# Kernel tuning notes

Hardware: AMD Instinct MI355X
Metric: run time of the kernel (lower is better)

Reference implementation:

```python
import jax, jax.numpy as jnp
import numpy as np

EMB = 768
HEADS = 12
HEAD_DIM = EMB // HEADS
LN_EPS = 1e-5


def _layernorm(x, g, b):
    mu = jnp.mean(x, axis=-1, keepdims=True)
    var = jnp.mean(jnp.square(x - mu), axis=-1, keepdims=True)
    return (x - mu) * jax.lax.rsqrt(var + LN_EPS) * g + b


def _att_block(x, ln_g, ln_b, w_qkv, b_qkv, w_proj, b_proj):
    # x: [b, n, e]
    B, N, E = x.shape
    h, d = HEADS, HEAD_DIM
    qkv = _layernorm(x, ln_g, ln_b) @ w_qkv.T + b_qkv          # [b, n, 3e]
    # einops 'b n (h d qkv)': last axis factors as (h, d, 3), qkv innermost
    qkv = qkv.reshape(B, N, h, d, 3)
    qkv = jnp.moveaxis(qkv, (4, 2), (0, 2))                    # [3, b, h, n, d]
    q, k, v = qkv[0], qkv[1], qkv[2]
    scale = d ** (-0.5)
    # NOTE: original code DIVIDES by scale (= multiplies by sqrt(d)) -- faithful
    scores = jnp.einsum('bhqd,bhkd->bhqk', q, k) / scale       # [b, h, n, n]
    attn = jax.nn.softmax(scores, axis=-1)
    out = jnp.einsum('bhqk,bhkd->bhqd', attn, v)               # [b, h, n, d]
    out = out.transpose(0, 2, 1, 3).reshape(B, N, E)           # [b, n, e]
    return x + out @ w_proj.T + b_proj


def setup_inputs() -> dict:
    key = jax.random.key(0)
    ks = jax.random.split(key, 8)
    B, N, E = 2, 2048, EMB
    s = E ** (-0.5)
    return {
        'modal1': jax.random.normal(ks[0], (B, N, E), jnp.float32),
        'modal2': jax.random.normal(ks[1], (B, N, E), jnp.float32),
        'ln1_g': jnp.ones((E,), jnp.float32),
        'ln1_b': jnp.zeros((E,), jnp.float32),
        'w_qkv1': jax.random.normal(ks[2], (3 * E, E), jnp.float32) * s,
        'b_qkv1': jnp.zeros((3 * E,), jnp.float32),
        'w_proj1': jax.random.normal(ks[3], (E, E), jnp.float32) * s,
        'b_proj1': jnp.zeros((E,), jnp.float32),
        'ln2_g': jnp.ones((E,), jnp.float32),
        'ln2_b': jnp.zeros((E,), jnp.float32),
        'w_qkv2': jax.random.normal(ks[4], (3 * E, E), jnp.float32) * s,
        'b_qkv2': jnp.zeros((3 * E,), jnp.float32),
        'w_proj2': jax.random.normal(ks[5], (E, E), jnp.float32) * s,
        'b_proj2': jnp.zeros((E,), jnp.float32),
    }


def reference(modal1, modal2, ln1_g, ln1_b, w_qkv1, b_qkv1, w_proj1, b_proj1,
              ln2_g, ln2_b, w_qkv2, b_qkv2, w_proj2, b_proj2):
    out1 = _att_block(modal1, ln1_g, ln1_b, w_qkv1, b_qkv1, w_proj1, b_proj1)
    out2 = _att_block(modal2, ln2_g, ln2_b, w_qkv2, b_qkv2, w_proj2, b_proj2)
    return (out1, out2)
```

## Files before the change

kernel.cpp:

```cpp
#include <hip/hip_runtime.h>
#include <hip/hip_bf16.h>


typedef unsigned short u16;
typedef unsigned int   u32;
typedef __attribute__((ext_vector_type(4)))  float floatx4;
typedef __attribute__((ext_vector_type(16))) float floatx16;
typedef __attribute__((ext_vector_type(8)))  short shortx8;
typedef __attribute__((ext_vector_type(2)))  unsigned int uintx2;

#define EMB   768
#define SEQ   2048
#define NHEAD 12
#define HDIM  64
#define RPM   4096
#define NROW  8192
#define NUNIT 48
#define KTS   4096
#define CS_SCALE 11.5415603271f

__device__ __forceinline__ float bf2f(u16 h) {
  union { u32 u; float f; } v; v.u = ((u32)h) << 16; return v.f;
}
__device__ __forceinline__ u16 f2bf(float f) {
  union { float f; u32 u; } v; v.f = f;
  u32 r = v.u + 0x7fffu + ((v.u >> 16) & 1u);
  return (u16)(r >> 16);
}
__device__ __forceinline__ u32 cvtpk_bf16(float a, float b) {
  u32 r;
  asm("v_cvt_pk_bf16_f32 %0, %1, %2" : "=v"(r) : "v"(a), "v"(b));
  return r;
}
__device__ __forceinline__ void swap_halves(u32 a, u32 b, u32& x, u32& y) {
#if __has_builtin(__builtin_amdgcn_permlane32_swap)
  uintx2 r = __builtin_amdgcn_permlane32_swap(a, b, false, false);
  x = r.x; y = r.y;
#else
  u32 ax = (u32)__shfl_xor((int)a, 32);
  u32 bx = (u32)__shfl_xor((int)b, 32);
  bool h = (threadIdx.x & 32) != 0;
  x = h ? bx : a;
  y = h ? b : ax;
#endif
}

__global__ __launch_bounds__(256) void k_pre(
    const float* __restrict__ wq1, const float* __restrict__ wq2,
    u16* __restrict__ wh, u16* __restrict__ wl,
    const float* __restrict__ x1, const float* __restrict__ x2,
    const float* __restrict__ g1, const float* __restrict__ b1,
    const float* __restrict__ g2, const float* __restrict__ b2,
    u16* __restrict__ xn_hi, u16* __restrict__ xn_lo)
{
  int bx = blockIdx.x;
  int t = threadIdx.x;
  if (bx < 4608) {
    int modal = bx / 2304, rowp = bx % 2304;
    int typ = rowp / 768, hd = rowp % 768;
    const float* W = (modal ? wq2 : wq1) + (size_t)(hd * 3 + typ) * EMB;
    size_t dst = (size_t)bx * EMB;
    #pragma unroll
    for (int i = 0; i < 3; ++i) {
      int e = t + i * 256;
      float v = W[e];
      u16 h = f2bf(v);
      wh[dst + e] = h;
      wl[dst + e] = f2bf(v - bf2f(h));
    }
  } else {
    int row = bx - 4608;
    int modal = row >> 12;
    const float* x = modal ? x2 : x1;
    const float* g = modal ? g2 : g1;
    const float* bb = modal ? b2 : b1;
    int r = row & (RPM - 1);
    const float* xr = x + (size_t)r * EMB;
    float v0 = xr[t], v1 = xr[t + 256], v2 = xr[t + 512];
    float s = v0 + v1 + v2;
    float s2 = v0 * v0 + v1 * v1 + v2 * v2;
    #pragma unroll
    for (int m = 1; m < 64; m <<= 1) { s += __shfl_xor(s, m); s2 += __shfl_xor(s2, m); }
    __shared__ float ls[4], ls2[4];
    int w = t >> 6;
    if ((t & 63) == 0) { ls[w] = s; ls2[w] = s2; }
    __syncthreads();
    s = ls[0] + ls[1] + ls[2] + ls[3];
    s2 = ls2[0] + ls2[1] + ls2[2] + ls2[3];
    float mu = s * (1.0f / EMB);
    float var = s2 * (1.0f / EMB) - mu * mu;
    float rs = rsqrtf(var + 1e-5f);
    size_t base = (size_t)row * EMB;
    float vv[3] = { v0, v1, v2 };
    #pragma unroll
    for (int i = 0; i < 3; ++i) {
      int e = t + i * 256;
      float xn = (vv[i] - mu) * rs * g[e] + bb[e];
      u16 h = f2bf(xn);
      xn_hi[base + e] = h;
      xn_lo[base + e] = f2bf(xn - bf2f(h));
    }
  }
}

__global__ __launch_bounds__(256) void prep_wp(
    const float* __restrict__ wp1, const float* __restrict__ wp2,
    u16* __restrict__ wh)
{
  int bx = blockIdx.x;
  int modal = bx / 768, row = bx % 768;
  const float* W = (modal ? wp2 : wp1) + (size_t)row * EMB;
  size_t dst = (size_t)bx * EMB;
  int t = threadIdx.x;
  #pragma unroll
  for (int i = 0; i < 3; ++i) {
    int e = t + i * 256;
    wh[dst + e] = f2bf(W[e]);
  }
}

__global__ __launch_bounds__(256) void k_qkv(
    const u16* __restrict__ xn_hi, const u16* __restrict__ xn_lo,
    const u16* __restrict__ wqh, const u16* __restrict__ wql,
    const float* __restrict__ bq1, const float* __restrict__ bq2,
    u16* __restrict__ q_hi, u16* __restrict__ q_lo,
    u16* __restrict__ k_hi, u16* __restrict__ k_lo,
    u16* __restrict__ vT)
{
  int mt = blockIdx.x, ntile = blockIdx.y, modal = blockIdx.z;
  const float* BQ = modal ? bq2 : bq1;
  int typ = ntile / 6;
  int hd0 = (ntile % 6) * 128;

  __shared__ __align__(16) u16 As_hi[2][128 * 32], Wh[2][128 * 32],
                               As_lo[2][128 * 32], Wl[2][128 * 32];

  int tid = threadIdx.x, lane = tid & 63, w = tid >> 6;
  int wm = (w >> 1) * 64, wn = (w & 1) * 64;
  int lc = lane & 15, lq = lane >> 4;

  int srow = lane >> 2;
  int schunk = ((lane & 3) ^ (srow & 3)) << 3;

  floatx4 acc[4][4] = {};
  const u16* aH = xn_hi + (size_t)(modal * RPM + mt * 128) * EMB;
  const u16* aL = xn_lo + (size_t)(modal * RPM + mt * 128) * EMB;
  const u16* wH = wqh + (size_t)(modal * 2304 + typ * 768 + hd0) * EMB;
  const u16* wL = wql + (size_t)(modal * 2304 + typ * 768 + hd0) * EMB;

  auto stage = [&](int buf, int k0) {
    if (typ != 2) {
      #pragma unroll
      for (int c = 0; c < 8; ++c) {
        int seg = w * 8 + c;
        int tile = seg >> 3, segin = seg & 7;
        size_t off = (size_t)(segin * 16 + srow) * EMB + k0 + schunk;
        const u16* src; u16* dstb;
        if (tile == 0)      { src = aH + off; dstb = &As_hi[buf][0]; }
        else if (tile == 1) { src = wH + off; dstb = &Wh[buf][0]; }
        else if (tile == 2) { src = aL + off; dstb = &As_lo[buf][0]; }
        else                { src = wL + off; dstb = &Wl[buf][0]; }
        __builtin_amdgcn_global_load_lds(
            (const __attribute__((address_space(1))) unsigned int*)src,
            (__attribute__((address_space(3))) unsigned int*)(dstb + segin * 512), 16, 0, 0);
      }
    } else {
      #pragma unroll
      for (int c = 0; c < 4; ++c) {
        int seg = w * 4 + c;
        int tile = seg >> 3, segin = seg & 7;
        size_t off = (size_t)(segin * 16 + srow) * EMB + k0 + schunk;
        const u16* src; u16* dstb;
        if (tile == 0) { src = aH + off; dstb = &As_hi[buf][0]; }
        else           { src = wH + off; dstb = &Wh[buf][0]; }
        __builtin_amdgcn_global_load_lds(
            (const __attribute__((address_space(1))) unsigned int*)src,
            (__attribute__((address_space(3))) unsigned int*)(dstb + segin * 512), 16, 0, 0);
      }
    }
  };

  stage(0, 0);
  for (int kk = 0; kk < 24; ++kk) {
    int cur = kk & 1;
    bool more = (kk + 1 < 24);
    if (more) stage(cur ^ 1, (kk + 1) * 32);
    if (typ != 2) {
      if (more) asm volatile("s_waitcnt vmcnt(8)" ::: "memory");
      else      asm volatile("s_waitcnt vmcnt(0)" ::: "memory");
    } else {
      if (more) asm volatile("s_waitcnt vmcnt(4)" ::: "memory");
      else      asm volatile("s_waitcnt vmcnt(0)" ::: "memory");
    }
    __builtin_amdgcn_s_barrier();
    __builtin_amdgcn_sched_barrier(0);

    shortx8 ah[4], al[4], whf[4], wlf[4];
    int rsw = lc & 3;
    int ca = (lq ^ rsw) << 3;
    #pragma unroll
    for (int i = 0; i < 4; ++i) {
      int ra = wm + i * 16 + lc, rw = wn + i * 16 + lc;
      ah[i]  = *(const shortx8*)&As_hi[cur][ra * 32 + ca];
      whf[i] = *(const shortx8*)&Wh[cur][rw * 32 + ca];
      if (typ != 2) {
        al[i]  = *(const shortx8*)&As_lo[cur][ra * 32 + ca];
        wlf[i] = *(const shortx8*)&Wl[cur][rw * 32 + ca];
      }
    }
    #pragma unroll
    for (int i = 0; i < 4; ++i)
      #pragma unroll
      for (int jn = 0; jn < 4; ++jn) {
        acc[i][jn] = __builtin_amdgcn_mfma_f32_16x16x32_bf16(ah[i], whf[jn], acc[i][jn], 0, 0, 0);
        if (typ != 2) {
          acc[i][jn] = __builtin_amdgcn_mfma_f32_16x16x32_bf16(al[i], whf[jn], acc[i][jn], 0, 0, 0);
          acc[i][jn] = __builtin_amdgcn_mfma_f32_16x16x32_bf16(ah[i], wlf[jn], acc[i][jn], 0, 0, 0);
        }
      }
    asm volatile("s_waitcnt lgkmcnt(0)" ::: "memory");
    __builtin_amdgcn_s_barrier();
    __builtin_amdgcn_sched_barrier(0);
  }

  #pragma unroll
  for (int i = 0; i < 4; ++i) {
    int mrow0 = mt * 128 + wm + i * 16 + lq * 4;
    #pragma unroll
    for (int jn = 0; jn < 4; ++jn) {
      int colp = hd0 + wn + jn * 16 + lc;
      int h = colp >> 6, d = colp & 63;
      float bias = BQ[colp * 3 + typ];
      #pragma unroll
      for (int r = 0; r < 4; ++r) {
        int mrow = mrow0 + r;
        int b = mrow >> 11, nq = mrow & (SEQ - 1);
        int uu = modal * 24 + b * 12 + h;
        float val = acc[i][jn][r] + bias;
        if (typ == 0) {
          val *= CS_SCALE;
          size_t o = ((size_t)uu * SEQ + nq) * HDIM + d;
          u16 hh = f2bf(val); q_hi[o] = hh; q_lo[o] = f2bf(val - bf2f(hh));
        } else if (typ == 1) {
          size_t o = ((size_t)uu * SEQ + nq) * HDIM + d;
          u16 hh = f2bf(val); k_hi[o] = hh; k_lo[o] = f2bf(val - bf2f(hh));
        } else {
          vT[((size_t)uu * HDIM + d) * SEQ + nq] = f2bf(val);
        }
      }
    }
  }
}

__global__ __launch_bounds__(256, 3) void k_attn(
    const u16* __restrict__ q_hi, const u16* __restrict__ q_lo,
    const u16* __restrict__ k_hi, const u16* __restrict__ k_lo,
    const u16* __restrict__ vT, u16* __restrict__ attn_out)
{
  int id = blockIdx.x + (blockIdx.y << 4);
  int xcd = id & 7, j = id >> 3;
  int u = xcd * 6 + (j >> 4);
  int qt = j & 15;

  __shared__ __align__(16) u16 lds[2][3 * KTS];

  int tid = threadIdx.x, lane = tid & 63, w = tid >> 6;
  int col = lane & 31, hi = lane >> 5;
  int swz = (col & 7) << 4;

  shortx8 qh[4], qlo[4];
  {
    size_t qb = ((size_t)u * SEQ + qt * 128 + w * 32 + col) * HDIM + hi * 8;
    #pragma unroll
    for (int s = 0; s < 4; ++s) {
      qh[s]  = *(const shortx8*)(q_hi + qb + s * 16);
      qlo[s] = *(const shortx8*)(q_lo + qb + s * 16);
    }
  }

  int lrow = lane >> 3;
  int lcol = ((lane & 7) ^ lrow) << 3;
  const u16* kh_src = k_hi + (size_t)u * SEQ * HDIM;
  const u16* kl_src = k_lo + (size_t)u * SEQ * HDIM;
  const u16* v_src  = vT  + (size_t)u * HDIM * SEQ;

  auto stage = [&](int buf, int kc) {
    #pragma unroll
    for (int c = 0; c < 6; ++c) {
      int seg = w * 6 + c;
      int tile = seg >> 3, segin = seg & 7;
      u16* dst = &lds[buf][tile * KTS + segin * 512];
      const u16* src;
      if (tile == 0)      src = kh_src + (size_t)(kc + segin * 8 + lrow) * HDIM + lcol;
      else if (tile == 1) src = kl_src + (size_t)(kc + segin * 8 + lrow) * HDIM + lcol;
      else                src = v_src  + (size_t)(segin * 8 + lrow) * SEQ + kc + lcol;
      __builtin_amdgcn_global_load_lds(
          (const __attribute__((address_space(1))) unsigned int*)src,
          (__attribute__((address_space(3))) unsigned int*)dst, 16, 0, 0);
    }
  };

  floatx16 O0 = {}, O1 = {};
  float m_r = -1e30f, lsum = 0.0f;
  const float THR = 8.0f;

  stage(0, 0);
  __syncthreads();

  for (int t = 0; t < SEQ / 64; ++t) {
    int cur = t & 1;
    if (t + 1 < SEQ / 64) stage(cur ^ 1, (t + 1) * 64);

    const char* Kh = (const char*)&lds[cur][0];
    const char* Kl = (const char*)&lds[cur][KTS];
    const char* Vt = (const char*)&lds[cur][2 * KTS];

    floatx16 S0 = {}, S1 = {};
    __builtin_amdgcn_s_setprio(1);
    #pragma unroll
    for (int s = 0; s < 4; ++s) {
      int cb = (s * 32 + hi * 16) ^ swz;
      shortx8 kf0 = *(const shortx8*)(Kh + col * 128 + cb);
      shortx8 kl0 = *(const shortx8*)(Kl + col * 128 + cb);
      shortx8 kf1 = *(const shortx8*)(Kh + (32 + col) * 128 + cb);
      shortx8 kl1 = *(const shortx8*)(Kl + (32 + col) * 128 + cb);
      S0 = __builtin_amdgcn_mfma_f32_32x32x16_bf16(kf0, qh[s],  S0, 0, 0, 0);
      S1 = __builtin_amdgcn_mfma_f32_32x32x16_bf16(kf1, qh[s],  S1, 0, 0, 0);
      S0 = __builtin_amdgcn_mfma_f32_32x32x16_bf16(kf0, qlo[s], S0, 0, 0, 0);
      S1 = __builtin_amdgcn_mfma_f32_32x32x16_bf16(kf1, qlo[s], S1, 0, 0, 0);
      S0 = __builtin_amdgcn_mfma_f32_32x32x16_bf16(kl0, qh[s],  S0, 0, 0, 0);
      S1 = __builtin_amdgcn_mfma_f32_32x32x16_bf16(kl1, qh[s],  S1, 0, 0, 0);
    }
    __builtin_amdgcn_s_setprio(0);

    float tm[16];
    #pragma unroll
    for (int r = 0; r < 16; ++r) tm[r] = fmaxf(S0[r], S1[r]);
    #pragma unroll
    for (int st = 8; st >= 1; st >>= 1)
      #pragma unroll
      for (int i = 0; i < st; ++i) tm[i] = fmaxf(tm[i], tm[i + st]);
    float mx = tm[0];
    mx = fmaxf(mx, __shfl_xor(mx, 32));

    if (!__all(mx <= m_r + THR)) {
      float mn = fmaxf(m_r, mx);
      float alpha = __builtin_amdgcn_exp2f(m_r - mn);
      m_r = mn;
      lsum *= alpha;
      #pragma unroll
      for (int r = 0; r < 16; ++r) {
        int qsrc = (r & 3) + 8 * (r >> 2) + 4 * hi;
        union { float f; int i; } a; a.f = alpha;
        a.i = __builtin_amdgcn_ds_bpermute(qsrc << 2, a.i);
        O0[r] *= a.f; O1[r] *= a.f;
      }
    }

    __builtin_amdgcn_s_setprio(1);
    #pragma unroll
    for (int ks = 0; ks < 4; ++ks) {
      const int h2 = ks & 1;
      float ee[8];
      #pragma unroll
      for (int i = 0; i < 8; ++i) {
        float sv = (ks < 2) ? S0[h2 * 8 + i] : S1[h2 * 8 + i];
        ee[i] = __builtin_amdgcn_exp2f(sv - m_r);
      }
      lsum += ((ee[0] + ee[1]) + (ee[2] + ee[3])) + ((ee[4] + ee[5]) + (ee[6] + ee[7]));
      u32 A = cvtpk_bf16(ee[0], ee[1]);
      u32 B = cvtpk_bf16(ee[2], ee[3]);
      u32 C = cvtpk_bf16(ee[4], ee[5]);
      u32 D = cvtpk_bf16(ee[6], ee[7]);
      u32 w0, w1, w2, w3;
      swap_halves(A, C, w0, w2);
      swap_halves(B, D, w1, w3);
      union { u32 uu[4]; shortx8 ss; } pk_;
      pk_.uu[0] = w0; pk_.uu[1] = w1; pk_.uu[2] = w2; pk_.uu[3] = w3;
      int cb = (ks * 32 + hi * 16) ^ swz;
      shortx8 v0 = *(const shortx8*)(Vt + col * 128 + cb);
      shortx8 v1 = *(const shortx8*)(Vt + (32 + col) * 128 + cb);
      O0 = __builtin_amdgcn_mfma_f32_32x32x16_bf16(pk_.ss, v0, O0, 0, 0, 0);
      O1 = __builtin_amdgcn_mfma_f32_32x32x16_bf16(pk_.ss, v1, O1, 0, 0, 0);
    }
    __builtin_amdgcn_s_setprio(0);

    __syncthreads();
  }

  float lt = lsum + __shfl_xor(lsum, 32);
  float rl = __builtin_amdgcn_rcpf(lt);
  int modal = u / 24, b = (u / 12) & 1, h = u % 12;
  size_t obase = ((size_t)(modal * RPM + b * SEQ + qt * 128 + w * 32)) * EMB + h * 64 + col;
  #pragma unroll
  for (int r = 0; r < 16; ++r) {
    int ql_ = (r & 3) + 8 * (r >> 2) + 4 * hi;
    union { float f; int i; } a; a.f = rl;
    a.i = __builtin_amdgcn_ds_bpermute(ql_ << 2, a.i);
    size_t ob = obase + (size_t)ql_ * EMB;
    attn_out[ob]      = f2bf(O0[r] * a.f);
    attn_out[ob + 32] = f2bf(O1[r] * a.f);
  }
}

__global__ __launch_bounds__(256) void k_proj(
    const u16* __restrict__ ao, const u16* __restrict__ wph,
    const float* __restrict__ x1, const float* __restrict__ x2,
    const float* __restrict__ bp1, const float* __restrict__ bp2,
    float* __restrict__ out)
{
  int mt = blockIdx.x, ntile = blockIdx.y, modal = blockIdx.z;
  const float* BP = modal ? bp2 : bp1;
  const float* x  = modal ? x2 : x1;

  __shared__ __align__(16) u16 As[2][64 * 32], Ws[2][128 * 32];
  int tid = threadIdx.x, lane = tid & 63, w = tid >> 6;
  int wm = (w >> 1) * 32, wn = (w & 1) * 64;
  int lc = lane & 15, lq = lane >> 4;

  int srow = lane >> 2;
  int schunk = ((lane & 3) ^ (srow & 3)) << 3;

  floatx4 acc[2][4] = {};
  const u16* aP = ao  + (size_t)(modal * RPM + mt * 64) * EMB;
  const u16* wP = wph + (size_t)(modal * 768 + ntile * 128) * EMB;

  auto stage = [&](int buf, int k0) {
    #pragma unroll
    for (int c = 0; c < 3; ++c) {
      int seg = w * 3 + c;
      const u16* src; u16* dst;
      if (seg < 4) {
        src = aP + (size_t)(seg * 16 + srow) * EMB + k0 + schunk;
        dst = &As[buf][0] + seg * 512;
      } else {
        int s2 = seg - 4;
        src = wP + (size_t)(s2 * 16 + srow) * EMB + k0 + schunk;
        dst = &Ws[buf][0] + s2 * 512;
      }
      __builtin_amdgcn_global_load_lds(
          (const __attribute__((address_space(1))) unsigned int*)src,
          (__attribute__((address_space(3))) unsigned int*)dst, 16, 0, 0);
    }
  };

  stage(0, 0);
  for (int kk = 0; kk < 24; ++kk) {
    int cur = kk & 1;
    bool more = (kk + 1 < 24);
    if (more) stage(cur ^ 1, (kk + 1) * 32);
    if (more) asm volatile("s_waitcnt vmcnt(3)" ::: "memory");
    else      asm volatile("s_waitcnt vmcnt(0)" ::: "memory");
    __builtin_amdgcn_s_barrier();
    __builtin_amdgcn_sched_barrier(0);

    int ca = (lq ^ (lc & 3)) << 3;
    shortx8 af[2], wf[4];
    #pragma unroll
    for (int i = 0; i < 2; ++i) af[i] = *(const shortx8*)&As[cur][(wm + i * 16 + lc) * 32 + ca];
    #pragma unroll
    for (int i = 0; i < 4; ++i) wf[i] = *(const shortx8*)&Ws[cur][(wn + i * 16 + lc) * 32 + ca];
    #pragma unroll
    for (int i = 0; i < 2; ++i)
      #pragma unroll
      for (int jn = 0; jn < 4; ++jn)
        acc[i][jn] = __builtin_amdgcn_mfma_f32_16x16x32_bf16(af[i], wf[jn], acc[i][jn], 0, 0, 0);
    asm volatile("s_waitcnt lgkmcnt(0)" ::: "memory");
    __builtin_amdgcn_s_barrier();
    __builtin_amdgcn_sched_barrier(0);
  }

  #pragma unroll
  for (int i = 0; i < 2; ++i) {
    int mrow0 = mt * 64 + wm + i * 16 + lq * 4;
    #pragma unroll
    for (int jn = 0; jn < 4; ++jn) {
      int col = ntile * 128 + wn + jn * 16 + lc;
      float bias = BP[col];
      #pragma unroll
      for (int r = 0; r < 4; ++r) {
        int mrow = mrow0 + r;
        float val = acc[i][jn][r] + bias + x[(size_t)mrow * EMB + col];
        out[((size_t)(modal * RPM + mrow)) * EMB + col] = val;
      }
    }
  }
}

extern "C" void kernel_launch(void* const* d_in, const int* in_sizes, int n_in,
                              void* d_out, int out_size, void* d_ws, size_t ws_size,
                              hipStream_t stream) {
  const float* modal1 = (const float*)d_in[0];
  const float* modal2 = (const float*)d_in[1];
  const float* ln1_g  = (const float*)d_in[2];
  const float* ln1_b  = (const float*)d_in[3];
  const float* w_qkv1 = (const float*)d_in[4];
  const float* b_qkv1 = (const float*)d_in[5];
  const float* w_proj1= (const float*)d_in[6];
  const float* b_proj1= (const float*)d_in[7];
  const float* ln2_g  = (const float*)d_in[8];
  const float* ln2_b  = (const float*)d_in[9];
  const float* w_qkv2 = (const float*)d_in[10];
  const float* b_qkv2 = (const float*)d_in[11];
  const float* w_proj2= (const float*)d_in[12];
  const float* b_proj2= (const float*)d_in[13];
  float* out = (float*)d_out;

  const size_t BUFE = (size_t)NROW * EMB;
  const size_t WQE  = (size_t)2 * 2304 * EMB;
  u16* xn_hi = (u16*)d_ws;
  u16* xn_lo = xn_hi + BUFE;
  u16* q_hi  = xn_lo + BUFE;
  u16* q_lo  = q_hi + BUFE;
  u16* k_hi  = q_lo + BUFE;
  u16* k_lo  = k_hi + BUFE;
  u16* vT    = k_lo + BUFE;
  u16* wq_h  = vT + BUFE;
  u16* wq_l  = wq_h + WQE;
  u16* attn  = xn_hi;
  u16* wp_h  = q_lo;

  k_pre<<<4608 + NROW, 256, 0, stream>>>(w_qkv1, w_qkv2, wq_h, wq_l,
                                         modal1, modal2, ln1_g, ln1_b, ln2_g, ln2_b,
                                         xn_hi, xn_lo);
  dim3 g2(32, 18, 2);
  k_qkv<<<g2, 256, 0, stream>>>(xn_hi, xn_lo, wq_h, wq_l, b_qkv1, b_qkv2,
                                q_hi, q_lo, k_hi, k_lo, vT);
  dim3 g3(16, 48);
  k_attn<<<g3, 256, 0, stream>>>(q_hi, q_lo, k_hi, k_lo, vT, attn);
  prep_wp<<<1536, 256, 0, stream>>>(w_proj1, w_proj2, wp_h);
  dim3 g4(64, 6, 2);
  k_proj<<<g4, 256, 0, stream>>>(attn, wp_h, modal1, modal2, b_proj1, b_proj2, out);
}
```

Before: 345.2 us.

## Load QKV activation operands directly to registers, stage only weights in LDS

The QKV GEMM kernel no longer stages the activation hi/lo tiles through shared memory. Each wave loads its A fragments straight from global memory into registers, prefetched one k-step ahead, and only the weight tiles go through LDS via global_load_lds. This halves LDS footprint and LDS read traffic, which may improve occupancy. The cost is that A rows shared by the two waves along the N dimension are now fetched from global twice, and the extra in-flight register prefetch raises register pressure.

```diff
diff --git a/kernel.cpp b/kernel.cpp
--- a/kernel.cpp
+++ b/kernel.cpp
@@ -132,8 +132,7 @@
   int typ = ntile / 6;
   int hd0 = (ntile % 6) * 128;
 
-  __shared__ __align__(16) u16 As_hi[2][128 * 32], Wh[2][128 * 32],
-                               As_lo[2][128 * 32], Wl[2][128 * 32];
+  __shared__ __align__(16) u16 Wh[2][128 * 32], Wl[2][128 * 32];
 
   int tid = threadIdx.x, lane = tid & 63, w = tid >> 6;
   int wm = (w >> 1) * 64, wn = (w & 1) * 64;
@@ -148,65 +147,68 @@
   const u16* wH = wqh + (size_t)(modal * 2304 + typ * 768 + hd0) * EMB;
   const u16* wL = wql + (size_t)(modal * 2304 + typ * 768 + hd0) * EMB;
 
-  auto stage = [&](int buf, int k0) {
+  auto stageW = [&](int buf, int k0) {
     if (typ != 2) {
-      #pragma unroll
-      for (int c = 0; c < 8; ++c) {
-        int seg = w * 8 + c;
-        int tile = seg >> 3, segin = seg & 7;
-        size_t off = (size_t)(segin * 16 + srow) * EMB + k0 + schunk;
-        const u16* src; u16* dstb;
-        if (tile == 0)      { src = aH + off; dstb = &As_hi[buf][0]; }
-        else if (tile == 1) { src = wH + off; dstb = &Wh[buf][0]; }
-        else if (tile == 2) { src = aL + off; dstb = &As_lo[buf][0]; }
-        else                { src = wL + off; dstb = &Wl[buf][0]; }
-        __builtin_amdgcn_global_load_lds(
-            (const __attribute__((address_space(1))) unsigned int*)src,
-            (__attribute__((address_space(3))) unsigned int*)(dstb + segin * 512), 16, 0, 0);
-      }
-    } else {
       #pragma unroll
       for (int c = 0; c < 4; ++c) {
         int seg = w * 4 + c;
-        int tile = seg >> 3, segin = seg & 7;
+        const u16* src; u16* dstb; int segin;
+        if (seg < 8) { segin = seg;     src = wH; dstb = &Wh[buf][0]; }
+        else         { segin = seg - 8; src = wL; dstb = &Wl[buf][0]; }
         size_t off = (size_t)(segin * 16 + srow) * EMB + k0 + schunk;
-        const u16* src; u16* dstb;
-        if (tile == 0) { src = aH + off; dstb = &As_hi[buf][0]; }
-        else           { src = wH + off; dstb = &Wh[buf][0]; }
         __builtin_amdgcn_global_load_lds(
-            (const __attribute__((address_space(1))) unsigned int*)src,
+            (const __attribute__((address_space(1))) unsigned int*)(src + off),
             (__attribute__((address_space(3))) unsigned int*)(dstb + segin * 512), 16, 0, 0);
       }
+    } else {
+      #pragma unroll
+      for (int c = 0; c < 2; ++c) {
+        int seg = w * 2 + c;
+        size_t off = (size_t)(seg * 16 + srow) * EMB + k0 + schunk;
+        __builtin_amdgcn_global_load_lds(
+            (const __attribute__((address_space(1))) unsigned int*)(wH + off),
+            (__attribute__((address_space(3))) unsigned int*)(&Wh[buf][0] + seg * 512), 16, 0, 0);
+      }
     }
   };
 
-  stage(0, 0);
+  size_t abase = (size_t)(wm + lc) * EMB + lq * 8;
+  shortx8 ahN[4], alN[4];
+  auto loadA = [&](int k0) {
+    #pragma unroll
+    for (int i = 0; i < 4; ++i) {
+      size_t o = abase + (size_t)(i * 16) * EMB + k0;
+      ahN[i] = *(const shortx8*)(aH + o);
+      if (typ != 2) alN[i] = *(const shortx8*)(aL + o);
+    }
+  };
+
+  loadA(0);
+  stageW(0, 0);
   for (int kk = 0; kk < 24; ++kk) {
     int cur = kk & 1;
     bool more = (kk + 1 < 24);
-    if (more) stage(cur ^ 1, (kk + 1) * 32);
+    shortx8 ah[4], al[4];
+    #pragma unroll
+    for (int i = 0; i < 4; ++i) { ah[i] = ahN[i]; if (typ != 2) al[i] = alN[i]; }
+    if (more) { loadA((kk + 1) * 32); stageW(cur ^ 1, (kk + 1) * 32); }
     if (typ != 2) {
-      if (more) asm volatile("s_waitcnt vmcnt(8)" ::: "memory");
+      if (more) asm volatile("s_waitcnt vmcnt(12)" ::: "memory");
       else      asm volatile("s_waitcnt vmcnt(0)" ::: "memory");
     } else {
-      if (more) asm volatile("s_waitcnt vmcnt(4)" ::: "memory");
+      if (more) asm volatile("s_waitcnt vmcnt(6)" ::: "memory");
       else      asm volatile("s_waitcnt vmcnt(0)" ::: "memory");
     }
     __builtin_amdgcn_s_barrier();
     __builtin_amdgcn_sched_barrier(0);
 
-    shortx8 ah[4], al[4], whf[4], wlf[4];
-    int rsw = lc & 3;
-    int ca = (lq ^ rsw) << 3;
+    int ca = (lq ^ (lc & 3)) << 3;
+    shortx8 whf[4], wlf[4];
     #pragma unroll
     for (int i = 0; i < 4; ++i) {
-      int ra = wm + i * 16 + lc, rw = wn + i * 16 + lc;
-      ah[i]  = *(const shortx8*)&As_hi[cur][ra * 32 + ca];
+      int rw = wn + i * 16 + lc;
       whf[i] = *(const shortx8*)&Wh[cur][rw * 32 + ca];
-      if (typ != 2) {
-        al[i]  = *(const shortx8*)&As_lo[cur][ra * 32 + ca];
-        wlf[i] = *(const shortx8*)&Wl[cur][rw * 32 + ca];
-      }
+      if (typ != 2) wlf[i] = *(const shortx8*)&Wl[cur][rw * 32 + ca];
     }
     #pragma unroll
     for (int i = 0; i < 4; ++i)
```

Result: slower. 437.1 us (+26.6%).
